# Kernel optimization log

Hardware: AMD Instinct MI355X
Metric: run time of the kernel (lower is better)

Reference implementation:

```python
import jax, jax.numpy as jnp
import numpy as np

N = 8192        # points
M = 131072      # query-key pairs (edges)
C_IN = 512
H = 8           # heads
D = 64          # head_channels
BINS = 48
BIN_SIZE = 0.05


def setup_inputs() -> dict:
    key = jax.random.key(0)
    ks = jax.random.split(key, 8)
    x_F = jax.random.normal(ks[0], (N, C_IN), dtype=jnp.float32)
    x_C = jax.random.uniform(ks[1], (N, 3), dtype=jnp.float32)
    qk_pair_idxs = jax.random.randint(ks[2], (2, M), 0, N, dtype=jnp.int64)
    W_qkv = jax.random.normal(ks[3], (C_IN, 3 * H * D), dtype=jnp.float32) * 0.02
    b_qkv = jnp.zeros((3 * H * D,), dtype=jnp.float32)
    q_tables = jax.random.normal(ks[4], (3, BINS, H, D), dtype=jnp.float32) * 0.02
    k_tables = jax.random.normal(ks[5], (3, BINS, H, D), dtype=jnp.float32) * 0.02
    v_tables = jax.random.normal(ks[6], (3, BINS, H, D), dtype=jnp.float32) * 0.02
    return {"x_F": x_F, "x_C": x_C, "qk_pair_idxs": qk_pair_idxs,
            "W_qkv": W_qkv, "b_qkv": b_qkv,
            "q_tables": q_tables, "k_tables": k_tables, "v_tables": v_tables}


def reference(x_F, x_C, qk_pair_idxs, W_qkv, b_qkv, q_tables, k_tables, v_tables):
    n = x_F.shape[0]
    qkv = (x_F @ W_qkv + b_qkv).reshape(n, 3, H, D)
    q = qkv[:, 0] * (D ** -0.5)   # scale folded into queries, as in the module
    k = qkv[:, 1]
    v = qkv[:, 2]
    qi = qk_pair_idxs[0]
    ki = qk_pair_idxs[1]
    # quantized relative coordinates -> table bin indices [M,3]
    rel = (x_C[qi] - x_C[ki]) / BIN_SIZE + BINS / 2
    idx = jnp.clip(rel.astype(jnp.int32), 0, BINS - 1)
    # precompute per-point, per-axis, per-bin table dot products [N,3,BINS,H]
    q_dot = jnp.einsum('nhd,abhd->nabh', q, q_tables)
    k_dot = jnp.einsum('nhd,abhd->nabh', k, k_tables)
    # content logits [M,H]
    logits = jnp.einsum('mhd,mhd->mh', q[qi], k[ki])
    for a in range(3):  # fixed xyz axes
        logits = logits + q_dot[qi, a, idx[:, a]] + k_dot[ki, a, idx[:, a]]
    # scatter softmax over query index (per head)
    seg_max = jax.ops.segment_max(logits, qi, num_segments=n)
    e = jnp.exp(logits - seg_max[qi])
    denom = jax.ops.segment_sum(e, qi, num_segments=n)
    attn = e / denom[qi]  # [M,H]
    # value-side relative position bias, summed over axes [M,H,D]
    vt = v_tables[0, idx[:, 0]] + v_tables[1, idx[:, 1]] + v_tables[2, idx[:, 2]]
    contrib = attn[:, :, None] * (v[ki] + vt)            # [M,H,D]
    agg = jax.ops.segment_sum(contrib, qi, num_segments=n)  # [N,H,D]
    return agg.reshape(n, H * D)
```

## Files before the change

### kernel.cpp

```cpp
#include <hip/hip_runtime.h>
#include <hip/hip_bf16.h>
#include <stdint.h>

#define N_PTS 8192
#define M_EDGES 131072
#define CIN 512
#define QKV_COLS 1536

typedef __bf16 bf16x8 __attribute__((ext_vector_type(8)));
typedef float f32x4 __attribute__((ext_vector_type(4)));

#define GAS __attribute__((address_space(1)))
#define LAS __attribute__((address_space(3)))

__device__ __forceinline__ void gload_lds16(const void* g, void* l) {
  __builtin_amdgcn_global_load_lds((const GAS void*)g, (LAS void*)l, 16, 0, 0);
}

__global__ __launch_bounds__(256) void prep_kernel(
    const float* __restrict__ xF, const float* __restrict__ W,
    const float* __restrict__ qt, const float* __restrict__ kt,
    const float* __restrict__ vt, const int* __restrict__ pairs,
    const float* __restrict__ xc,
    __bf16* __restrict__ A, __bf16* __restrict__ BT,
    __bf16* __restrict__ qtb, __bf16* __restrict__ ktb, __bf16* __restrict__ vtT,
    int* __restrict__ qi_a, unsigned* __restrict__ pack0, int* __restrict__ cnt) {
  __shared__ float tile[32][33];
  int b = blockIdx.x;
  int tid = threadIdx.x;
  if (b < 4096) {
    int base = (b * 256 + tid) * 4;
    float4 v = *(const float4*)(xF + base);
    A[base + 0] = (__bf16)v.x;
    A[base + 1] = (__bf16)v.y;
    A[base + 2] = (__bf16)v.z;
    A[base + 3] = (__bf16)v.w;
  } else if (b < 4864) {
    int blk = b - 4096;
    int bk = blk & 15, bn = blk >> 4;
    int x = tid & 31, y = tid >> 5;
#pragma unroll
    for (int j = 0; j < 4; j++) {
      int r = y + j * 8;
      tile[r][x] = W[(size_t)(bk * 32 + r) * QKV_COLS + bn * 32 + x];
    }
    __syncthreads();
#pragma unroll
    for (int j = 0; j < 4; j++) {
      int r = y + j * 8;
      BT[(size_t)(bn * 32 + r) * CIN + bk * 32 + x] = (__bf16)tile[x][r];
    }
  } else if (b < 5152) {
    int i = (b - 4864) * 256 + tid;
    int d = i & 63, h = (i >> 6) & 7, ab = i >> 9;
    int po = (h * 144 + ab) * 64 + d;
    qtb[po] = (__bf16)qt[i];
    ktb[po] = (__bf16)kt[i];
  } else if (b < 5472) {
    int i = (b - 5152) * 256 + tid;
    int p = i % 160;
    int d = (i / 160) & 63;
    int h = i / 10240;
    vtT[i] = (p < 144) ? (__bf16)vt[p * 512 + h * 64 + d] : (__bf16)0.f;
  } else {
    int m = (b - 5472) * 256 + tid;
    int qi = pairs[m], ki = pairs[M_EDGES + m];
    unsigned pb = 0;
#pragma unroll
    for (int a = 0; a < 3; a++) {
      float rel = (xc[qi * 3 + a] - xc[ki * 3 + a]) / 0.05f + 24.0f;
      int bb = (int)rel;
      bb = bb < 0 ? 0 : (bb > 47 ? 47 : bb);
      pb |= (unsigned)bb << (6 * a);
    }
    qi_a[m] = qi;
    pack0[m] = (unsigned)ki | (pb << 13);
    atomicAdd(&cnt[qi], 1);
  }
}

__global__ __launch_bounds__(256) void gemm_scan_kernel(
    const __bf16* __restrict__ A, const __bf16* __restrict__ BT,
    const float* __restrict__ bias, __bf16* __restrict__ qb,
    __bf16* __restrict__ kv,
    const int* __restrict__ cnt, int* __restrict__ off, int* __restrict__ cursor,
    int* __restrict__ qperm) {
  __shared__ __align__(16) char At[2][64 * 128];
  __shared__ __align__(16) char Bt[2][128 * 128];
  __shared__ int wsum[4];
  __shared__ int hist2[64];
  __shared__ int bpos[64];
  int bid = blockIdx.x;
  int tid = threadIdx.x;

  if (bid == 1536) {
    int lane = tid & 63, w = tid >> 6;
    int local[32];
    int s = 0;
#pragma unroll
    for (int i = 0; i < 8; i++) {
      int4 v = ((const int4*)cnt)[tid * 8 + i];
      local[i * 4 + 0] = v.x; local[i * 4 + 1] = v.y;
      local[i * 4 + 2] = v.z; local[i * 4 + 3] = v.w;
      s += v.x + v.y + v.z + v.w;
    }
    int incl = s;
#pragma unroll
    for (int d = 1; d < 64; d <<= 1) {
      int t = __shfl_up(incl, d, 64);
      if (lane >= d) incl += t;
    }
    if (lane == 63) wsum[w] = incl;
    if (tid < 64) hist2[tid] = 0;
    __syncthreads();
    int woff = 0;
#pragma unroll
    for (int j = 0; j < 4; j++) woff += (j < w) ? wsum[j] : 0;
    int run = woff + incl - s;
    int base = tid * 32;
#pragma unroll
    for (int i = 0; i < 32; i++) {
      off[base + i] = run;
      cursor[base + i] = run;
      run += local[i];
      int c = local[i] < 63 ? local[i] : 63;
      atomicAdd(&hist2[c], 1);
    }
    if (tid == 255) off[N_PTS] = run;
    __syncthreads();
    if (tid < 64) {
      int p = 0;
      for (int bb = 63; bb > tid; bb--) p += hist2[bb];
      bpos[tid] = p;
    }
    __syncthreads();
#pragma unroll
    for (int i = 0; i < 32; i++) {
      int c = local[i] < 63 ? local[i] : 63;
      int pos = atomicAdd(&bpos[c], 1);
      qperm[pos] = base + i;
    }
    return;
  }

  int bn = bid % 12, bm = bid / 12;
  int w = tid >> 6, l = tid & 63;
  int wm = w & 1, wn = w >> 1;
  f32x4 acc[2][4] = {};
  const char* Ab = (const char*)A;
  const char* Bb = (const char*)BT;
  int lr = l & 15;
  int lk = (l >> 4) * 16;
  int xr = (lr & 7) << 4;

  auto stage = [&](int tk, int buf) {
#pragma unroll
    for (int r = 0; r < 2; r++) {
      int flat = r * 4096 + tid * 16;
      int row = flat >> 7, colb = flat & 127;
      int gcolb = colb ^ ((row & 7) << 4);
      gload_lds16(Ab + ((size_t)(bm * 64 + row) * CIN + tk * 64) * 2 + gcolb,
                  At[buf] + r * 4096 + w * 1024);
    }
#pragma unroll
    for (int r = 0; r < 4; r++) {
      int flat = r * 4096 + tid * 16;
      int row = flat >> 7, colb = flat & 127;
      int gcolb = colb ^ ((row & 7) << 4);
      gload_lds16(Bb + ((size_t)(bn * 128 + row) * CIN + tk * 64) * 2 + gcolb,
                  Bt[buf] + r * 4096 + w * 1024);
    }
  };

  stage(0, 0);
  __syncthreads();
  int cur = 0;
  for (int kt = 0; kt < 8; kt++) {
    if (kt < 7) stage(kt + 1, cur ^ 1);
#pragma unroll
    for (int ks = 0; ks < 2; ks++) {
      bf16x8 af[2], bfr[4];
      int cs = (ks * 64 + lk) ^ xr;
#pragma unroll
      for (int mf = 0; mf < 2; mf++) af[mf] = *(const bf16x8*)(At[cur] + (wm * 32 + mf * 16 + lr) * 128 + cs);
#pragma unroll
      for (int nf = 0; nf < 4; nf++) bfr[nf] = *(const bf16x8*)(Bt[cur] + (wn * 64 + nf * 16 + lr) * 128 + cs);
#pragma unroll
      for (int mf = 0; mf < 2; mf++)
#pragma unroll
        for (int nf = 0; nf < 4; nf++)
          acc[mf][nf] = __builtin_amdgcn_mfma_f32_16x16x32_bf16(af[mf], bfr[nf], acc[mf][nf], 0, 0, 0);
    }
    __syncthreads();
    cur ^= 1;
  }

  int lg = l >> 4;
#pragma unroll
  for (int mf = 0; mf < 2; mf++) {
#pragma unroll
    for (int nf = 0; nf < 4; nf++) {
      int gc = bn * 128 + wn * 64 + nf * 16 + lr;
      float b = bias[gc];
      int which = gc >> 9;
      int col = gc & 511;
      float scale = which == 0 ? 0.125f : 1.0f;
#pragma unroll
      for (int j = 0; j < 4; j++) {
        int gr = bm * 64 + wm * 32 + mf * 16 + lg * 4 + j;
        float val = (acc[mf][nf][j] + b) * scale;
        if (which == 0) qb[(size_t)gr * 512 + col] = (__bf16)val;
        else kv[(size_t)gr * 1024 + (which == 2 ? 512 : 0) + col] = (__bf16)val;
      }
    }
  }
}

__global__ __launch_bounds__(256) void td_scatter_kernel(
    const __bf16* __restrict__ qb, const __bf16* __restrict__ kv,
    const __bf16* __restrict__ qtb, const __bf16* __restrict__ ktb,
    __bf16* __restrict__ qdot, __bf16* __restrict__ kdot,
    const int* __restrict__ qi_a, const unsigned* __restrict__ pack0,
    int* __restrict__ cursor, unsigned* __restrict__ epack) {
  __shared__ __align__(16) char As[128 * 128];
  __shared__ __align__(16) char Bs[144 * 128];
  int bid = blockIdx.x;
  int tid = threadIdx.x;

  if (bid < 512) {
    int m = bid * 256 + tid;
    int qi = qi_a[m];
    int pos = atomicAdd(&cursor[qi], 1);
    epack[pos] = pack0[m];
    return;
  }

  int td = bid - 512;
  int nt = td & 63, h = (td >> 6) & 7, z = td >> 9;
  const __bf16* src = z ? kv : qb;
  const __bf16* tab = z ? ktb : qtb;
  __bf16* out = z ? kdot : qdot;
  size_t SB = z ? 2048 : 1024;
  int w = tid >> 6, l = tid & 63;
  const char* sb = (const char*)src;
  const char* tb = (const char*)tab + (size_t)h * 144 * 128;
#pragma unroll
  for (int p = 0; p < 4; p++) {
    int flat = p * 4096 + tid * 16;
    int row = flat >> 7, colb = flat & 127;
    int gcolb = colb ^ ((row & 7) << 4);
    gload_lds16(sb + (size_t)(nt * 128 + row) * SB + h * 128 + gcolb, As + p * 4096 + w * 1024);
    gload_lds16(tb + row * 128 + gcolb, Bs + p * 4096 + w * 1024);
  }
  if (w < 2) {
    int flat = 16384 + w * 1024 + l * 16;
    int row = flat >> 7, colb = flat & 127;
    int gcolb = colb ^ ((row & 7) << 4);
    gload_lds16(tb + row * 128 + gcolb, Bs + 16384 + w * 1024);
  }
  __syncthreads();

  f32x4 acc[2][9] = {};
  int lr = l & 15, lk = (l >> 4) * 16;
  int xr = (lr & 7) << 4;
#pragma unroll
  for (int ks = 0; ks < 2; ks++) {
    bf16x8 af[2], bf[9];
    int cs = (ks * 64 + lk) ^ xr;
#pragma unroll
    for (int mf = 0; mf < 2; mf++)
      af[mf] = *(const bf16x8*)(As + (w * 32 + mf * 16 + lr) * 128 + cs);
#pragma unroll
    for (int nf = 0; nf < 9; nf++)
      bf[nf] = *(const bf16x8*)(Bs + (nf * 16 + lr) * 128 + cs);
#pragma unroll
    for (int mf = 0; mf < 2; mf++)
#pragma unroll
      for (int nf = 0; nf < 9; nf++)
        acc[mf][nf] = __builtin_amdgcn_mfma_f32_16x16x32_bf16(af[mf], bf[nf], acc[mf][nf], 0, 0, 0);
  }

  int lg = l >> 4;
#pragma unroll
  for (int mf = 0; mf < 2; mf++)
#pragma unroll
    for (int nf = 0; nf < 9; nf++)
#pragma unroll
      for (int j = 0; j < 4; j++) {
        int n = nt * 128 + w * 32 + mf * 16 + lg * 4 + j;
        int ab = nf * 16 + lr;
        out[(size_t)n * 1152 + ab * 8 + h] = (__bf16)acc[mf][nf][j];
      }
}

__global__ __launch_bounds__(256) void attn_kernel(
    const __bf16* __restrict__ qb, const __bf16* __restrict__ kv,
    const __bf16* __restrict__ qdot, const __bf16* __restrict__ kdot,
    const int* __restrict__ off, const unsigned* __restrict__ epack,
    const int* __restrict__ qperm,
    __bf16* __restrict__ numb, float* __restrict__ den, __bf16* __restrict__ Hb) {
  __shared__ float hist[8 * 164];
  __shared__ float part[4][512];
  __shared__ float dpart[4][8];
  int n = qperm[blockIdx.x];
  int tid = threadIdx.x;
  int w = tid >> 6, l = tid & 63;
  int h = l >> 3, dg = l & 7;

  for (int i = tid; i < 8 * 164; i += 256) hist[i] = 0.f;
  __syncthreads();

  bf16x8 q8 = *(const bf16x8*)(qb + (n << 9) + l * 8);
  float qv[8];
#pragma unroll
  for (int j = 0; j < 8; j++) qv[j] = (float)q8[j];

  float acc[8] = {0.f, 0.f, 0.f, 0.f, 0.f, 0.f, 0.f, 0.f};
  float dn = 0.f;
  int e0 = off[n], e1 = off[n + 1];
  const __bf16* qd_row = qdot + (size_t)n * 1152;
  int axis = dg < 3 ? dg : dg - 3;
  int tsh = 6 * axis;

  int e = e0 + w;
  unsigned pk_next = (e < e1) ? epack[__builtin_amdgcn_readfirstlane(e)] : 0u;
  for (; e < e1; e += 4) {
    unsigned pk = pk_next;
    int en = e + 4;
    if (en < e1) pk_next = epack[__builtin_amdgcn_readfirstlane(en)];
    int ki = pk & 8191;
    unsigned pb = pk >> 13;
    bf16x8 k8 = *(const bf16x8*)(kv + ((size_t)ki << 10) + l * 8);
    bf16x8 v8 = *(const bf16x8*)(kv + ((size_t)ki << 10) + 512 + l * 8);
    int bin = (int)((pb >> tsh) & 63u);
    int idx = (axis * 48 + bin) * 8 + h;
    const __bf16* tbl = dg < 3 ? qd_row : (kdot + (size_t)ki * 1152);
    float p = (dg < 6) ? (float)tbl[idx] : 0.f;
#pragma unroll
    for (int j = 0; j < 8; j++) p += qv[j] * (float)k8[j];
    p += __shfl_xor(p, 1, 64);
    p += __shfl_xor(p, 2, 64);
    p += __shfl_xor(p, 4, 64);
    float x = __expf(p);
    dn += x;
#pragma unroll
    for (int j = 0; j < 8; j++) acc[j] += x * (float)v8[j];
    if (dg == 0) {
      float* hh = hist + h * 164;
      atomicAdd(hh + (pb & 63), x);
      atomicAdd(hh + 48 + ((pb >> 6) & 63), x);
      atomicAdd(hh + 96 + ((pb >> 12) & 63), x);
    }
  }

  f32x4 a0 = {acc[0], acc[1], acc[2], acc[3]};
  f32x4 a1 = {acc[4], acc[5], acc[6], acc[7]};
  *(f32x4*)&part[w][l * 8] = a0;
  *(f32x4*)&part[w][l * 8 + 4] = a1;
  if (dg == 0) dpart[w][h] = dn;
  __syncthreads();

#pragma unroll
  for (int half = 0; half < 2; half++) {
    int idx = tid + half * 256;
    float s = part[0][idx] + part[1][idx] + part[2][idx] + part[3][idx];
    numb[(n << 9) + idx] = (__bf16)s;
  }
  if (tid < 8) {
    den[n * 8 + tid] = dpart[0][tid] + dpart[1][tid] + dpart[2][tid] + dpart[3][tid];
  }
  for (int i = tid; i < 1280; i += 256) {
    int hh = i / 160, p = i % 160;
    Hb[(size_t)n * 1280 + i] = (__bf16)hist[hh * 164 + p];
  }
}

__global__ __launch_bounds__(256) void finish_kernel(const __bf16* __restrict__ Hb,
                                                     const __bf16* __restrict__ vtT,
                                                     const __bf16* __restrict__ numb,
                                                     const float* __restrict__ den,
                                                     float* __restrict__ out) {
  __shared__ __align__(16) char As[2][128 * 64];
  __shared__ __align__(16) char Bs[2][64 * 64];
  int nt = blockIdx.x, h = blockIdx.y;
  int tid = threadIdx.x, w = tid >> 6, l = tid & 63;
  int lr = l & 15, lk = (l >> 4) * 16;
  int xr = (lr & 3) << 4;
  const char* Ab = (const char*)Hb;
  const char* Bb = (const char*)vtT;
  f32x4 acc[2][4] = {};

  auto stage = [&](int tk, int buf) {
#pragma unroll
    for (int c = 0; c < 2; c++) {
      int flat = c * 4096 + tid * 16;
      int row = flat >> 6, colb = flat & 63;
      int gcolb = colb ^ ((row & 3) << 4);
      gload_lds16(Ab + ((size_t)(nt * 128 + row) * 1280 + h * 160 + tk * 32) * 2 + gcolb,
                  As[buf] + c * 4096 + w * 1024);
    }
    {
      int flat = tid * 16;
      int row = flat >> 6, colb = flat & 63;
      int gcolb = colb ^ ((row & 3) << 4);
      gload_lds16(Bb + ((size_t)(h * 64 + row) * 160 + tk * 32) * 2 + gcolb,
                  Bs[buf] + w * 1024);
    }
  };

  stage(0, 0);
  __syncthreads();
  int cur = 0;
  for (int kt = 0; kt < 5; kt++) {
    if (kt < 4) stage(kt + 1, cur ^ 1);
    bf16x8 af[2], bf[4];
    int cs = lk ^ xr;
#pragma unroll
    for (int mf = 0; mf < 2; mf++) af[mf] = *(const bf16x8*)(As[cur] + (w * 32 + mf * 16 + lr) * 64 + cs);
#pragma unroll
    for (int nf = 0; nf < 4; nf++) bf[nf] = *(const bf16x8*)(Bs[cur] + (nf * 16 + lr) * 64 + cs);
#pragma unroll
    for (int mf = 0; mf < 2; mf++)
#pragma unroll
      for (int nf = 0; nf < 4; nf++)
        acc[mf][nf] = __builtin_amdgcn_mfma_f32_16x16x32_bf16(af[mf], bf[nf], acc[mf][nf], 0, 0, 0);
    __syncthreads();
    cur ^= 1;
  }

  int lg = l >> 4;
#pragma unroll
  for (int mf = 0; mf < 2; mf++) {
#pragma unroll
    for (int j = 0; j < 4; j++) {
      int n = nt * 128 + w * 32 + mf * 16 + lg * 4 + j;
      float dnv = den[n * 8 + h];
      float inv = dnv > 0.f ? 1.f / dnv : 0.f;
#pragma unroll
      for (int nf = 0; nf < 4; nf++) {
        int gi = (n << 9) + h * 64 + nf * 16 + lr;
        out[gi] = ((float)numb[gi] + acc[mf][nf][j]) * inv;
      }
    }
  }
}

extern "C" void kernel_launch(void* const* d_in, const int* in_sizes, int n_in,
                              void* d_out, int out_size, void* d_ws, size_t ws_size,
                              hipStream_t stream) {
  const float* xF = (const float*)d_in[0];
  const float* xC = (const float*)d_in[1];
  const int* pairs = (const int*)d_in[2];
  const float* W = (const float*)d_in[3];
  const float* bias = (const float*)d_in[4];
  const float* qt = (const float*)d_in[5];
  const float* kt = (const float*)d_in[6];
  const float* vt = (const float*)d_in[7];
  float* out = (float*)d_out;

  char* ws = (char*)d_ws;
  size_t o = 0;
  auto alloc = [&](size_t bytes) {
    void* p = ws + o;
    o = (o + bytes + 255) & ~(size_t)255;
    return p;
  };
  char* region0 = (char*)alloc((size_t)N_PTS * 1280 * 2);
  __bf16* A = (__bf16*)region0;
  __bf16* BT = (__bf16*)(region0 + (size_t)N_PTS * CIN * 2);
  __bf16* Hb = (__bf16*)region0;
  __bf16* qb = (__bf16*)alloc((size_t)N_PTS * 512 * 2);
  __bf16* kv = (__bf16*)alloc((size_t)N_PTS * 1024 * 2);
  __bf16* qtb = (__bf16*)alloc((size_t)8 * 144 * 64 * 2);
  __bf16* ktb = (__bf16*)alloc((size_t)8 * 144 * 64 * 2);
  __bf16* vtT = (__bf16*)alloc((size_t)8 * 64 * 160 * 2);
  __bf16* qdot = (__bf16*)alloc((size_t)N_PTS * 1152 * 2);
  __bf16* kdot = (__bf16*)alloc((size_t)N_PTS * 1152 * 2);
  __bf16* numb = (__bf16*)alloc((size_t)N_PTS * 512 * 2);
  float* den = (float*)alloc((size_t)N_PTS * 8 * 4);
  int* qi_a = (int*)alloc(M_EDGES * 4);
  unsigned* pack0 = (unsigned*)alloc(M_EDGES * 4);
  unsigned* epack = (unsigned*)alloc(M_EDGES * 4);
  int* cnt = (int*)alloc(N_PTS * 4);
  int* off = (int*)alloc((N_PTS + 1) * 4);
  int* cursor = (int*)alloc(N_PTS * 4);
  int* qperm = (int*)alloc(N_PTS * 4);

  hipMemsetAsync(cnt, 0, N_PTS * 4, stream);

  prep_kernel<<<5984, 256, 0, stream>>>(xF, W, qt, kt, vt, pairs, xC,
                                        A, BT, qtb, ktb, vtT, qi_a, pack0, cnt);
  gemm_scan_kernel<<<1537, 256, 0, stream>>>(A, BT, bias, qb, kv, cnt, off, cursor, qperm);
  td_scatter_kernel<<<1536, 256, 0, stream>>>(qb, kv, qtb, ktb, qdot, kdot,
                                              qi_a, pack0, cursor, epack);
  attn_kernel<<<N_PTS, 256, 0, stream>>>(qb, kv, qdot, kdot, off, epack, qperm,
                                         numb, den, Hb);
  finish_kernel<<<dim3(N_PTS / 128, 8), 256, 0, stream>>>(Hb, vtT, numb, den, out);
}
```

Baseline: 145.2 us.

## Enlarge QKV GEMM tile to 128x128, drop double buffering, spread histogram atomics

The QKV projection GEMM tile grows from 64x128 to 128x128 per block. This halves the grid and doubles MFMA work per wave, giving more reuse of staged operands, but it drops the double-buffered LDS prefetch so loads are no longer overlapped with compute. In the attention kernel, the three per-axis histogram atomics are spread across three lanes instead of being issued serially by one lane. The histogram write-out is vectorised into 8-wide bf16 stores.

```diff
diff --git a/kernel.cpp b/kernel.cpp
--- a/kernel.cpp
+++ b/kernel.cpp
@@ -85,15 +85,15 @@
     __bf16* __restrict__ kv,
     const int* __restrict__ cnt, int* __restrict__ off, int* __restrict__ cursor,
     int* __restrict__ qperm) {
-  __shared__ __align__(16) char At[2][64 * 128];
-  __shared__ __align__(16) char Bt[2][128 * 128];
+  __shared__ __align__(16) char At[128 * 128];
+  __shared__ __align__(16) char Bt[128 * 128];
   __shared__ int wsum[4];
   __shared__ int hist2[64];
   __shared__ int bpos[64];
   int bid = blockIdx.x;
   int tid = threadIdx.x;
 
-  if (bid == 1536) {
+  if (bid == 768) {
     int lane = tid & 63, w = tid >> 6;
     int local[32];
     int s = 0;
@@ -146,58 +146,45 @@
   int bn = bid % 12, bm = bid / 12;
   int w = tid >> 6, l = tid & 63;
   int wm = w & 1, wn = w >> 1;
-  f32x4 acc[2][4] = {};
+  f32x4 acc[4][4] = {};
   const char* Ab = (const char*)A;
   const char* Bb = (const char*)BT;
   int lr = l & 15;
   int lk = (l >> 4) * 16;
   int xr = (lr & 7) << 4;
 
-  auto stage = [&](int tk, int buf) {
-#pragma unroll
-    for (int r = 0; r < 2; r++) {
-      int flat = r * 4096 + tid * 16;
-      int row = flat >> 7, colb = flat & 127;
-      int gcolb = colb ^ ((row & 7) << 4);
-      gload_lds16(Ab + ((size_t)(bm * 64 + row) * CIN + tk * 64) * 2 + gcolb,
-                  At[buf] + r * 4096 + w * 1024);
-    }
+  for (int kt = 0; kt < 8; kt++) {
 #pragma unroll
     for (int r = 0; r < 4; r++) {
       int flat = r * 4096 + tid * 16;
       int row = flat >> 7, colb = flat & 127;
       int gcolb = colb ^ ((row & 7) << 4);
-      gload_lds16(Bb + ((size_t)(bn * 128 + row) * CIN + tk * 64) * 2 + gcolb,
-                  Bt[buf] + r * 4096 + w * 1024);
-    }
-  };
-
-  stage(0, 0);
-  __syncthreads();
-  int cur = 0;
-  for (int kt = 0; kt < 8; kt++) {
-    if (kt < 7) stage(kt + 1, cur ^ 1);
+      gload_lds16(Ab + ((size_t)(bm * 128 + row) * CIN + kt * 64) * 2 + gcolb,
+                  At + r * 4096 + w * 1024);
+      gload_lds16(Bb + ((size_t)(bn * 128 + row) * CIN + kt * 64) * 2 + gcolb,
+                  Bt + r * 4096 + w * 1024);
+    }
+    __syncthreads();
 #pragma unroll
     for (int ks = 0; ks < 2; ks++) {
-      bf16x8 af[2], bfr[4];
+      bf16x8 af[4], bfr[4];
       int cs = (ks * 64 + lk) ^ xr;
 #pragma unroll
-      for (int mf = 0; mf < 2; mf++) af[mf] = *(const bf16x8*)(At[cur] + (wm * 32 + mf * 16 + lr) * 128 + cs);
-#pragma unroll
-      for (int nf = 0; nf < 4; nf++) bfr[nf] = *(const bf16x8*)(Bt[cur] + (wn * 64 + nf * 16 + lr) * 128 + cs);
-#pragma unroll
-      for (int mf = 0; mf < 2; mf++)
+      for (int mf = 0; mf < 4; mf++) af[mf] = *(const bf16x8*)(At + (wm * 64 + mf * 16 + lr) * 128 + cs);
+#pragma unroll
+      for (int nf = 0; nf < 4; nf++) bfr[nf] = *(const bf16x8*)(Bt + (wn * 64 + nf * 16 + lr) * 128 + cs);
+#pragma unroll
+      for (int mf = 0; mf < 4; mf++)
 #pragma unroll
         for (int nf = 0; nf < 4; nf++)
           acc[mf][nf] = __builtin_amdgcn_mfma_f32_16x16x32_bf16(af[mf], bfr[nf], acc[mf][nf], 0, 0, 0);
     }
     __syncthreads();
-    cur ^= 1;
   }
 
   int lg = l >> 4;
 #pragma unroll
-  for (int mf = 0; mf < 2; mf++) {
+  for (int mf = 0; mf < 4; mf++) {
 #pragma unroll
     for (int nf = 0; nf < 4; nf++) {
       int gc = bn * 128 + wn * 64 + nf * 16 + lr;
@@ -207,7 +194,7 @@
       float scale = which == 0 ? 0.125f : 1.0f;
 #pragma unroll
       for (int j = 0; j < 4; j++) {
-        int gr = bm * 64 + wm * 32 + mf * 16 + lg * 4 + j;
+        int gr = bm * 128 + wm * 64 + mf * 16 + lg * 4 + j;
         float val = (acc[mf][nf][j] + b) * scale;
         if (which == 0) qb[(size_t)gr * 512 + col] = (__bf16)val;
         else kv[(size_t)gr * 1024 + (which == 2 ? 512 : 0) + col] = (__bf16)val;
@@ -345,11 +332,8 @@
     dn += x;
 #pragma unroll
     for (int j = 0; j < 8; j++) acc[j] += x * (float)v8[j];
-    if (dg == 0) {
-      float* hh = hist + h * 164;
-      atomicAdd(hh + (pb & 63), x);
-      atomicAdd(hh + 48 + ((pb >> 6) & 63), x);
-      atomicAdd(hh + 96 + ((pb >> 12) & 63), x);
+    if (dg < 3) {
+      atomicAdd(hist + h * 164 + dg * 48 + (int)((pb >> (6 * dg)) & 63u), x);
     }
   }
 
@@ -369,9 +353,13 @@
   if (tid < 8) {
     den[n * 8 + tid] = dpart[0][tid] + dpart[1][tid] + dpart[2][tid] + dpart[3][tid];
   }
-  for (int i = tid; i < 1280; i += 256) {
-    int hh = i / 160, p = i % 160;
-    Hb[(size_t)n * 1280 + i] = (__bf16)hist[hh * 164 + p];
+  if (tid < 160) {
+    int row = tid / 20, p = (tid % 20) * 8;
+    const float* hp = hist + row * 164 + p;
+    bf16x8 o;
+#pragma unroll
+    for (int j = 0; j < 8; j++) o[j] = (__bf16)hp[j];
+    *(bf16x8*)(Hb + (size_t)n * 1280 + row * 160 + p) = o;
   }
 }
 
@@ -490,7 +478,7 @@
 
   prep_kernel<<<5984, 256, 0, stream>>>(xF, W, qt, kt, vt, pairs, xC,
                                         A, BT, qtb, ktb, vtT, qi_a, pack0, cnt);
-  gemm_scan_kernel<<<1537, 256, 0, stream>>>(A, BT, bias, qb, kv, cnt, off, cursor, qperm);
+  gemm_scan_kernel<<<769, 256, 0, stream>>>(A, BT, bias, qb, kv, cnt, off, cursor, qperm);
   td_scatter_kernel<<<1536, 256, 0, stream>>>(qb, kv, qtb, ktb, qdot, kdot,
                                               qi_a, pack0, cursor, epack);
   attn_kernel<<<N_PTS, 256, 0, stream>>>(qb, kv, qdot, kdot, off, epack, qperm,
```

Result: no change. 142.7 us (-1.8%).
